# Kernel tuning notes

Hardware: AMD Instinct MI355X
Metric: run time of the kernel (lower is better)

The kernel has to match this reference:

```python
import jax, jax.numpy as jnp
import numpy as np
from jax import lax

RATIO = 2.0
ITERATIONS = 1


def setup_inputs() -> dict:
    key = jax.random.key(0)
    k1, k2 = jax.random.split(key)
    N, H, W = 64, 512, 512
    x = jax.random.normal(k1, (N, H, W), dtype=jnp.float32)  # logits
    y = jax.random.randint(k2, (N, H, W), 0, 2, dtype=jnp.int32)  # binary labels
    return {"x": x, "y": y}


def _erode(m):
    # cv2.erode with 3x3 all-ones kernel == 3x3 min-pool; cv2 default border
    # value for erode is +inf, matching reduce_window's init_value padding.
    return lax.reduce_window(m, jnp.inf, lax.min, (1, 3, 3), (1, 1, 1), 'SAME')


def _dilate(m):
    # cv2.dilate == 3x3 max-pool; default border value -inf == init_value pad.
    return lax.reduce_window(m, -jnp.inf, lax.max, (1, 3, 3), (1, 1, 1), 'SAME')


def reference(x, y):
    yf = y.astype(x.dtype)
    # elementwise BCE-with-logits (reduction='none'), numerically stable
    loss = jnp.maximum(x, 0.0) - x * yf + jnp.log1p(jnp.exp(-jnp.abs(x)))
    m = (y > 0).astype(x.dtype)  # [N,H,W] binary mask
    ero, dil = m, m
    for _ in range(ITERATIONS):
        ero = _erode(ero)
        dil = _dilate(dil)
    border = dil - ero  # 1 on border pixels, 0 elsewhere
    w = border * RATIO + (1.0 - border)
    return (loss * w).mean()
```

## Files before the change

### kernel.cpp

```cpp
#include <hip/hip_runtime.h>
#include <math.h>

#define NIMG 64
#define HH 512
#define WW 512
#define TR 32
#define NSEG 8
#define LROWS (TR + 2)
#define NBLOCKS (NIMG * (HH / TR))
#define INV_TOTAL (1.0f / 16777216.0f)

__global__ __launch_bounds__(512) void border_loss_main(
    const float* __restrict__ x, const int* __restrict__ y,
    float* __restrict__ part, int atomic_mode)
{
    __shared__ unsigned long long mm[LROWS][NSEG];
    __shared__ unsigned long long mz[LROWS][NSEG];
    __shared__ float wsum[8];

    const int tid  = threadIdx.x;
    const int lane = tid & 63;
    const int w    = tid >> 6;
    const int nb   = blockIdx.x;
    const int n    = nb >> 4;
    const int R0   = (nb & 15) * TR;
    const long long imgbase = (long long)n * HH * WW;

    for (int T = w; T < LROWS * NSEG; T += 8) {
        int j = T >> 3;
        int s = T & 7;
        int gr = R0 - 1 + j;
        unsigned long long bm = 0ull, bz = 0ull;
        if ((unsigned)gr < (unsigned)HH) {
            int yv = y[imgbase + (long long)gr * WW + (s << 6) + lane];
            bm = __ballot(yv > 0);
            bz = ~bm;
        }
        if (lane == 0) { mm[j][s] = bm; mz[j][s] = bz; }
    }
    __syncthreads();

    float acc = 0.0f;
    #pragma unroll
    for (int k = 0; k < TR / 8; ++k) {
        int rr = w + (k << 3);
        int jr = rr + 1;
        const float* xrow = x + imgbase + (long long)(R0 + rr) * WW;

        unsigned long long vm_prev = 0ull, vz_prev = 0ull;
        unsigned long long vm_cur = mm[jr-1][0] | mm[jr][0] | mm[jr+1][0];
        unsigned long long vz_cur = mz[jr-1][0] | mz[jr][0] | mz[jr+1][0];

        #pragma unroll
        for (int s = 0; s < NSEG; ++s) {
            unsigned long long vm_next = 0ull, vz_next = 0ull;
            if (s + 1 < NSEG) {
                vm_next = mm[jr-1][s+1] | mm[jr][s+1] | mm[jr+1][s+1];
                vz_next = mz[jr-1][s+1] | mz[jr][s+1] | mz[jr+1][s+1];
            }
            unsigned long long hm = vm_cur | (vm_cur << 1) | (vm_cur >> 1)
                                  | (vm_prev >> 63) | (vm_next << 63);
            unsigned long long hz = vz_cur | (vz_cur << 1) | (vz_cur >> 1)
                                  | (vz_prev >> 63) | (vz_next << 63);
            unsigned long long border = hm & hz;
            unsigned long long mrow   = mm[jr][s];

            float xf = xrow[(s << 6) + lane];
            float a  = fabsf(xf);
            float lg = __logf(1.0f + __expf(-a));
            float mterm = ((mrow >> lane) & 1ull) ? xf : 0.0f;
            float loss  = fmaxf(xf, 0.0f) - mterm + lg;
            float wgt   = ((border >> lane) & 1ull) ? 2.0f : 1.0f;
            acc = fmaf(loss, wgt, acc);

            vm_prev = vm_cur; vz_prev = vz_cur;
            vm_cur  = vm_next; vz_cur  = vz_next;
        }
    }

    #pragma unroll
    for (int off = 32; off > 0; off >>= 1)
        acc += __shfl_down(acc, off);
    __syncthreads();
    if (lane == 0) wsum[w] = acc;
    __syncthreads();
    if (tid == 0) {
        float s = 0.0f;
        #pragma unroll
        for (int i = 0; i < 8; ++i) s += wsum[i];
        if (atomic_mode) atomicAdd(part, s * INV_TOTAL);
        else             part[blockIdx.x] = s;
    }
}

__global__ __launch_bounds__(256) void border_loss_reduce(
    const float* __restrict__ part, float* __restrict__ out)
{
    __shared__ float wsum[4];
    float s = 0.0f;
    for (int i = threadIdx.x; i < NBLOCKS; i += 256) s += part[i];
    #pragma unroll
    for (int off = 32; off > 0; off >>= 1)
        s += __shfl_down(s, off);
    if ((threadIdx.x & 63) == 0) wsum[threadIdx.x >> 6] = s;
    __syncthreads();
    if (threadIdx.x == 0)
        out[0] = (wsum[0] + wsum[1] + wsum[2] + wsum[3]) * INV_TOTAL;
}

__global__ void border_loss_zero(float* out) { out[0] = 0.0f; }

extern "C" void kernel_launch(void* const* d_in, const int* in_sizes, int n_in,
                              void* d_out, int out_size, void* d_ws, size_t ws_size,
                              hipStream_t stream)
{
    const float* x = (const float*)d_in[0];
    const int*   y = (const int*)d_in[1];
    float* out = (float*)d_out;

    if (ws_size >= (size_t)NBLOCKS * sizeof(float)) {
        float* part = (float*)d_ws;
        border_loss_main<<<NBLOCKS, 512, 0, stream>>>(x, y, part, 0);
        border_loss_reduce<<<1, 256, 0, stream>>>(part, out);
    } else {
        border_loss_zero<<<1, 1, 0, stream>>>(out);
        border_loss_main<<<NBLOCKS, 512, 0, stream>>>(x, y, out, 1);
    }
}
```

Before: 164.0 us.

## Stream rows per wave with register-rolling ballot masks instead of shared-memory staging

Each wave now owns one 64-column segment and walks down the 32-row strip. The top/center/bottom row masks are kept in registers as a rolling window, and neighbour-segment edge bits come from scalar (readfirstlane) loads. This removes the shared-memory mask tile, the block-wide barrier before compute, and the LDS reads in the inner loop. It also uses inverse_ballot when available to extract per-lane bits. In exchange, each row's y is loaded right before use, so there is less load batching, and the edge scalar loads add latency on the serial row chain.

```diff
diff --git a/kernel.cpp b/kernel.cpp
--- a/kernel.cpp
+++ b/kernel.cpp
@@ -4,92 +4,123 @@
 #define NIMG 64
 #define HH 512
 #define WW 512
-#define TR 32
+#define SH 32
 #define NSEG 8
-#define LROWS (TR + 2)
-#define NBLOCKS (NIMG * (HH / TR))
+#define NSTRIP (HH / SH)
+#define NBLOCKS (NIMG * NSTRIP)
 #define INV_TOTAL (1.0f / 16777216.0f)
 
-__global__ __launch_bounds__(512) void border_loss_main(
+typedef unsigned long long u64;
+
+#if defined(__has_builtin)
+#  if __has_builtin(__builtin_amdgcn_inverse_ballot_w64)
+#    define HAVE_INV_BALLOT 1
+#  endif
+#endif
+
+__device__ __forceinline__ int uload(const int* __restrict__ p, int idx) {
+    return p[__builtin_amdgcn_readfirstlane(idx)];
+}
+
+__global__ __launch_bounds__(512, 8) void border_loss_main(
     const float* __restrict__ x, const int* __restrict__ y,
     float* __restrict__ part, int atomic_mode)
 {
-    __shared__ unsigned long long mm[LROWS][NSEG];
-    __shared__ unsigned long long mz[LROWS][NSEG];
     __shared__ float wsum[8];
 
     const int tid  = threadIdx.x;
     const int lane = tid & 63;
-    const int w    = tid >> 6;
-    const int nb   = blockIdx.x;
-    const int n    = nb >> 4;
-    const int R0   = (nb & 15) * TR;
-    const long long imgbase = (long long)n * HH * WW;
+    const int s    = tid >> 6;
+    const int b    = blockIdx.x;
+    const int n    = b >> 4;
+    const int R0   = (b & 15) * SH;
+    const int col0 = s << 6;
+    const int ibase = n * (HH * WW) + col0;
+    const int*   __restrict__ yb = y + ibase;
+    const float* __restrict__ xb = x + ibase;
+    const bool hasL = (s > 0), hasR = (s < NSEG - 1);
 
-    for (int T = w; T < LROWS * NSEG; T += 8) {
-        int j = T >> 3;
-        int s = T & 7;
-        int gr = R0 - 1 + j;
-        unsigned long long bm = 0ull, bz = 0ull;
-        if ((unsigned)gr < (unsigned)HH) {
-            int yv = y[imgbase + (long long)gr * WW + (s << 6) + lane];
-            bm = __ballot(yv > 0);
-            bz = ~bm;
-        }
-        if (lane == 0) { mm[j][s] = bm; mz[j][s] = bz; }
+    u64 bm_t, bz_t, bm_c, bz_c;
+    int lm_t, lz_t, rm_t, rz_t;
+    int lm_c, lz_c, rm_c, rz_c;
+
+    if (R0 > 0) {
+        const int o = (R0 - 1) * WW;
+        int yv = yb[o + lane];
+        bm_t = __ballot(yv > 0);
+        bz_t = ~bm_t;
+        if (hasL) { int v = uload(yb, o - 1);  lm_t = v > 0; lz_t = !lm_t; }
+        else      { lm_t = 0; lz_t = 0; }
+        if (hasR) { int v = uload(yb, o + 64); rm_t = v > 0; rz_t = !rm_t; }
+        else      { rm_t = 0; rz_t = 0; }
+    } else { bm_t = 0; bz_t = 0; lm_t = lz_t = rm_t = rz_t = 0; }
+
+    {
+        const int o = R0 * WW;
+        int yv = yb[o + lane];
+        bm_c = __ballot(yv > 0);
+        bz_c = ~bm_c;
+        if (hasL) { int v = uload(yb, o - 1);  lm_c = v > 0; lz_c = !lm_c; }
+        else      { lm_c = 0; lz_c = 0; }
+        if (hasR) { int v = uload(yb, o + 64); rm_c = v > 0; rz_c = !rm_c; }
+        else      { rm_c = 0; rz_c = 0; }
     }
-    __syncthreads();
 
     float acc = 0.0f;
-    #pragma unroll
-    for (int k = 0; k < TR / 8; ++k) {
-        int rr = w + (k << 3);
-        int jr = rr + 1;
-        const float* xrow = x + imgbase + (long long)(R0 + rr) * WW;
+    #pragma unroll 4
+    for (int r = 0; r < SH; ++r) {
+        const int gr = R0 + r;
+        const float xf = xb[gr * WW + lane];
 
-        unsigned long long vm_prev = 0ull, vz_prev = 0ull;
-        unsigned long long vm_cur = mm[jr-1][0] | mm[jr][0] | mm[jr+1][0];
-        unsigned long long vz_cur = mz[jr-1][0] | mz[jr][0] | mz[jr+1][0];
+        u64 bm_b = 0, bz_b = 0;
+        int lm_b = 0, lz_b = 0, rm_b = 0, rz_b = 0;
+        const int gb = gr + 1;
+        if (gb < HH) {
+            const int o = gb * WW;
+            int yv = yb[o + lane];
+            bm_b = __ballot(yv > 0);
+            bz_b = ~bm_b;
+            if (hasL) { int v = uload(yb, o - 1);  lm_b = v > 0; lz_b = !lm_b; }
+            if (hasR) { int v = uload(yb, o + 64); rm_b = v > 0; rz_b = !rm_b; }
+        }
 
-        #pragma unroll
-        for (int s = 0; s < NSEG; ++s) {
-            unsigned long long vm_next = 0ull, vz_next = 0ull;
-            if (s + 1 < NSEG) {
-                vm_next = mm[jr-1][s+1] | mm[jr][s+1] | mm[jr+1][s+1];
-                vz_next = mz[jr-1][s+1] | mz[jr][s+1] | mz[jr+1][s+1];
-            }
-            unsigned long long hm = vm_cur | (vm_cur << 1) | (vm_cur >> 1)
-                                  | (vm_prev >> 63) | (vm_next << 63);
-            unsigned long long hz = vz_cur | (vz_cur << 1) | (vz_cur >> 1)
-                                  | (vz_prev >> 63) | (vz_next << 63);
-            unsigned long long border = hm & hz;
-            unsigned long long mrow   = mm[jr][s];
+        const u64 vm = bm_t | bm_c | bm_b;
+        const u64 vz = bz_t | bz_c | bz_b;
+        const u64 hm = vm | (vm << 1) | (vm >> 1)
+                     | (u64)(unsigned)(lm_t | lm_c | lm_b)
+                     | ((u64)(unsigned)(rm_t | rm_c | rm_b) << 63);
+        const u64 hz = vz | (vz << 1) | (vz >> 1)
+                     | (u64)(unsigned)(lz_t | lz_c | lz_b)
+                     | ((u64)(unsigned)(rz_t | rz_c | rz_b) << 63);
+        const u64 border = hm & hz;
 
-            float xf = xrow[(s << 6) + lane];
-            float a  = fabsf(xf);
-            float lg = __logf(1.0f + __expf(-a));
-            float mterm = ((mrow >> lane) & 1ull) ? xf : 0.0f;
-            float loss  = fmaxf(xf, 0.0f) - mterm + lg;
-            float wgt   = ((border >> lane) & 1ull) ? 2.0f : 1.0f;
-            acc = fmaf(loss, wgt, acc);
+        const float lg = __logf(1.0f + __expf(-fabsf(xf)));
+#ifdef HAVE_INV_BALLOT
+        const bool mbit = __builtin_amdgcn_inverse_ballot_w64(bm_c);
+        const bool wbit = __builtin_amdgcn_inverse_ballot_w64(border);
+#else
+        const bool mbit = (bm_c   >> lane) & 1ull;
+        const bool wbit = (border >> lane) & 1ull;
+#endif
+        const float loss = fmaxf(xf, 0.0f) - (mbit ? xf : 0.0f) + lg;
+        acc = fmaf(loss, wbit ? 2.0f : 1.0f, acc);
 
-            vm_prev = vm_cur; vz_prev = vz_cur;
-            vm_cur  = vm_next; vz_cur  = vz_next;
-        }
+        bm_t = bm_c; bz_t = bz_c; bm_c = bm_b; bz_c = bz_b;
+        lm_t = lm_c; lz_t = lz_c; lm_c = lm_b; lz_c = lz_b;
+        rm_t = rm_c; rz_t = rz_c; rm_c = rm_b; rz_c = rz_b;
     }
 
     #pragma unroll
     for (int off = 32; off > 0; off >>= 1)
         acc += __shfl_down(acc, off);
-    __syncthreads();
-    if (lane == 0) wsum[w] = acc;
+    if (lane == 0) wsum[s] = acc;
     __syncthreads();
     if (tid == 0) {
-        float s = 0.0f;
+        float t = 0.0f;
         #pragma unroll
-        for (int i = 0; i < 8; ++i) s += wsum[i];
-        if (atomic_mode) atomicAdd(part, s * INV_TOTAL);
-        else             part[blockIdx.x] = s;
+        for (int i = 0; i < 8; ++i) t += wsum[i];
+        if (atomic_mode) atomicAdd(part, t * INV_TOTAL);
+        else             part[blockIdx.x] = t;
     }
 }
 
@@ -97,12 +128,12 @@
     const float* __restrict__ part, float* __restrict__ out)
 {
     __shared__ float wsum[4];
-    float s = 0.0f;
-    for (int i = threadIdx.x; i < NBLOCKS; i += 256) s += part[i];
+    float t = 0.0f;
+    for (int i = threadIdx.x; i < NBLOCKS; i += 256) t += part[i];
     #pragma unroll
     for (int off = 32; off > 0; off >>= 1)
-        s += __shfl_down(s, off);
-    if ((threadIdx.x & 63) == 0) wsum[threadIdx.x >> 6] = s;
+        t += __shfl_down(t, off);
+    if ((threadIdx.x & 63) == 0) wsum[threadIdx.x >> 6] = t;
     __syncthreads();
     if (threadIdx.x == 0)
         out[0] = (wsum[0] + wsum[1] + wsum[2] + wsum[3]) * INV_TOTAL;
```

After: 175.7 us. 1.07x slower.
